# Kernel optimization log

Hardware: AMD Instinct MI355X
Metric: run time of the kernel (lower is better)

The kernel has to match this reference:

```python
import jax, jax.numpy as jnp
import numpy as np
import math

H = 16
LN_EPS = 1e-5


def setup_inputs() -> dict:
    key = jax.random.key(0)
    ks = jax.random.split(key, 12)
    D = 1024
    F = T = 2048
    S = 512
    inp = {
        "hidden_states": jax.random.normal(ks[0], (S, D), jnp.float32),
        "fpos": jax.random.randint(ks[1], (F,), 0, 512, jnp.int64 if jax.config.jax_enable_x64 else jnp.int32).astype(jnp.int32),
        "tpos": jax.random.randint(ks[2], (T,), 0, 512, jnp.int32),
        "Wq": jax.random.normal(ks[3], (D, D), jnp.float32) * 0.02,
        "Wk": jax.random.normal(ks[4], (D, D), jnp.float32) * 0.02,
        "Wcb": jax.random.normal(ks[5], (D, H), jnp.float32) * 0.02,
        "Wv": jax.random.normal(ks[6], (D, D), jnp.float32) * 0.02,
        "bv": jnp.zeros((D,), jnp.float32),
        "mixing": jax.random.normal(ks[7], (H, D), jnp.float32) * 0.2,
        "Wd": jax.random.normal(ks[8], (D, D), jnp.float32) * 0.02,
        "bd": jnp.zeros((D,), jnp.float32),
        "ln_gamma": jnp.ones((D,), jnp.float32),
        "ln_beta": jnp.zeros((D,), jnp.float32),
    }
    return inp


def reference(hidden_states, fpos, tpos, Wq, Wk, Wcb, Wv, bv, mixing, Wd, bd, ln_gamma, ln_beta):
    D = hidden_states.shape[-1]
    Dh = D // H
    scale = 1.0 / math.sqrt(D / H)  # attention_head_size = dim_key_query_all / num_heads

    fidx = fpos % 512
    tidx = tpos % 512
    from_seq = hidden_states[fidx]            # [F, D]
    to_seq = hidden_states[tidx]              # [T, D]

    q = from_seq @ Wq                          # [F, D]
    k = to_seq @ Wk                            # [T, D]

    # per-head query mixing: mixed_query[h, f, d] = q[f, d] * mixing[h, d]
    mixed_q = q[None, :, :] * mixing[:, None, :]          # [H, F, D]
    scores = jnp.einsum('hfd,td->hft', mixed_q, k)        # [H, F, T]

    # content bias: [T, H] -> broadcast over queries as [H, 1, T]
    cb = (to_seq @ Wcb).T                                 # [H, T]
    scores = (scores + cb[:, None, :]) * scale

    probs = jax.nn.softmax(scores, axis=-1)               # [H, F, T]

    v = (to_seq @ Wv + bv).reshape(-1, H, Dh).transpose(1, 0, 2)  # [H, T, Dh]
    ctx = jnp.matmul(probs, v)                             # [H, F, Dh]
    ctx = ctx.transpose(1, 0, 2).reshape(-1, D)            # [F, D]

    out = ctx @ Wd + bd                                    # [F, D]
    res = from_seq + out

    mu = jnp.mean(res, axis=-1, keepdims=True)
    var = jnp.var(res, axis=-1, keepdims=True)
    normed = (res - mu) / jnp.sqrt(var + LN_EPS)
    return normed * ln_gamma + ln_beta
```

## Files before the change

### kernel.cpp

```cpp
#include <hip/hip_runtime.h>
#include <stdint.h>
#include <math.h>

typedef float    f32x4 __attribute__((ext_vector_type(4)));
typedef float    f32x2 __attribute__((ext_vector_type(2)));
typedef short    s16x8 __attribute__((ext_vector_type(8)));
typedef short    s16x4 __attribute__((ext_vector_type(4)));
typedef unsigned u32x4 __attribute__((ext_vector_type(4)));

#define SCALE_LOG2E 0.1803368751839806f

__device__ __forceinline__ float bf2f(short s) {
  unsigned u = ((unsigned)(unsigned short)s) << 16;
  return __builtin_bit_cast(float, u);
}
__device__ __forceinline__ short f2bf(float f) {
  unsigned u = __builtin_bit_cast(unsigned, f);
  u = u + 0x7fffu + ((u >> 16) & 1u);
  return (short)(u >> 16);
}
__device__ __forceinline__ unsigned cvtpk(float lo, float hi) {
  unsigned r;
  asm("v_cvt_pk_bf16_f32 %0, %1, %2" : "=v"(r) : "v"(lo), "v"(hi));
  return r;
}
__device__ __forceinline__ void g2l16(const void* g, void* l) {
  __builtin_amdgcn_global_load_lds((const __attribute__((address_space(1))) void*)g,
                                   (__attribute__((address_space(3))) void*)l,
                                   16, 0, 0);
}
#define BARRIER() do { __builtin_amdgcn_s_barrier(); __builtin_amdgcn_sched_barrier(0); } while (0)
#define VMCNT(N)  asm volatile("s_waitcnt vmcnt(" #N ")" ::: "memory")
#define MFMA(a, b, c) __builtin_amdgcn_mfma_f32_16x16x32_bf16(a, b, c, 0, 0, 0)

__global__ void wtrans_kernel(const float* __restrict__ Wq, const float* __restrict__ Wk,
                              const float* __restrict__ Wv, const float* __restrict__ Wd,
                              short* __restrict__ WqT, short* __restrict__ WkT,
                              short* __restrict__ WvT, short* __restrict__ WdT) {
  __shared__ float tile[64][65];
  const float* src; short* dst;
  switch (blockIdx.z) {
    case 0: src = Wq; dst = WqT; break;
    case 1: src = Wk; dst = WkT; break;
    case 2: src = Wv; dst = WvT; break;
    default: src = Wd; dst = WdT; break;
  }
  int k0 = blockIdx.y * 64;
  int n0 = blockIdx.x * 64;
  int tid = threadIdx.x;
#pragma unroll
  for (int p = 0; p < 4; ++p) {
    int idx = p * 1024 + tid * 4;
    int r = idx >> 6, c = idx & 63;
    f32x4 v = *(const f32x4*)(src + (size_t)(k0 + r) * 1024 + n0 + c);
    tile[r][c + 0] = v[0]; tile[r][c + 1] = v[1];
    tile[r][c + 2] = v[2]; tile[r][c + 3] = v[3];
  }
  __syncthreads();
#pragma unroll
  for (int p = 0; p < 2; ++p) {
    int idx = p * 2048 + tid * 8;
    int r = idx >> 6, c = idx & 63;
    s16x8 o;
#pragma unroll
    for (int i = 0; i < 8; ++i) o[i] = f2bf(tile[c + i][r]);
    *(s16x8*)(dst + (size_t)(n0 + r) * 1024 + k0 + c) = o;
  }
}

__global__ void smallconv_kernel(const float* __restrict__ Wcb, const float* __restrict__ mixing,
                                 short* __restrict__ WcbT, short* __restrict__ mixbf) {
  int idx = blockIdx.x * 256 + threadIdx.x;
  if (idx < 16384) {
    int h = idx >> 10, d = idx & 1023;
    WcbT[idx] = f2bf(Wcb[d * 16 + h]);
  } else {
    int j = idx - 16384;
    mixbf[j] = f2bf(mixing[j] * SCALE_LOG2E);
  }
}

__global__ void gather_kernel(const float* __restrict__ hidden, const int* __restrict__ fpos,
                              const int* __restrict__ tpos, float* __restrict__ from_f,
                              short* __restrict__ from_bf, short* __restrict__ to_bf) {
  int row = blockIdx.x;
  int c = threadIdx.x * 4;
  if (blockIdx.y == 0) {
    int src = fpos[row] & 511;
    f32x4 v = *(const f32x4*)(hidden + (size_t)src * 1024 + c);
    *(f32x4*)(from_f + (size_t)row * 1024 + c) = v;
    s16x4 o;
#pragma unroll
    for (int i = 0; i < 4; ++i) o[i] = f2bf(v[i]);
    *(s16x4*)(from_bf + (size_t)row * 1024 + c) = o;
  } else {
    int src = tpos[row] & 511;
    f32x4 v = *(const f32x4*)(hidden + (size_t)src * 1024 + c);
    s16x4 o;
#pragma unroll
    for (int i = 0; i < 4; ++i) o[i] = f2bf(v[i]);
    *(s16x4*)(to_bf + (size_t)row * 1024 + c) = o;
  }
}

__global__ __launch_bounds__(256, 2)
void qkv_gemm(const short* __restrict__ from_bf, const short* __restrict__ to_bf,
              const short* __restrict__ WqT, const short* __restrict__ WkT,
              const short* __restrict__ WvT, const float* __restrict__ bv,
              short* __restrict__ q_swz, short* __restrict__ k_swz, short* __restrict__ vTs) {
  __shared__ __align__(16) short As[128][64];
  __shared__ __align__(16) short Bs[128][64];
  int mode = blockIdx.z;
  const short* A = (mode == 0) ? from_bf : to_bf;
  const short* B = (mode == 0) ? WqT : (mode == 1) ? WkT : WvT;
  int m0 = blockIdx.x * 128, n0 = blockIdx.y * 128;
  int tid = threadIdx.x;
  int w = tid >> 6, l = tid & 63;
  int wr = w >> 1, wc = w & 1;
  f32x4 acc[4][4] = {};
  for (int k0 = 0; k0 < 1024; k0 += 64) {
    __syncthreads();
#pragma unroll
    for (int i = 0; i < 4; ++i) {
      int off = i * 4096 + tid * 16;
      int r = off >> 7, cb_ = off & 127;
      g2l16(A + ((size_t)(m0 + r) << 10) + k0 + (cb_ >> 1), (short*)As + (off >> 1));
      g2l16(B + ((size_t)(n0 + r) << 10) + k0 + (cb_ >> 1), (short*)Bs + (off >> 1));
    }
    __syncthreads();
#pragma unroll
    for (int ks = 0; ks < 2; ++ks) {
      s16x8 af[4], bfr[4];
#pragma unroll
      for (int m = 0; m < 4; ++m)
        af[m] = *(const s16x8*)&As[wr * 64 + m * 16 + (l & 15)][ks * 32 + (l >> 4) * 8];
#pragma unroll
      for (int n = 0; n < 4; ++n)
        bfr[n] = *(const s16x8*)&Bs[wc * 64 + n * 16 + (l & 15)][ks * 32 + (l >> 4) * 8];
#pragma unroll
      for (int m = 0; m < 4; ++m)
#pragma unroll
        for (int n = 0; n < 4; ++n)
          acc[m][n] = MFMA(af[m], bfr[n], acc[m][n]);
    }
  }
  int lr = (l >> 4) * 4, lc = l & 15;
#pragma unroll
  for (int m = 0; m < 4; ++m)
#pragma unroll
    for (int n = 0; n < 4; ++n) {
      int row = m0 + wr * 64 + m * 16 + lr;
      int col = n0 + wc * 64 + n * 16 + lc;
      if (mode == 0) {
#pragma unroll
        for (int r = 0; r < 4; ++r) {
          int rr = row + r;
          q_swz[(size_t)rr * 1024 + (col ^ ((rr & 7) << 3))] = f2bf(acc[m][n][r]);
        }
      } else if (mode == 1) {
#pragma unroll
        for (int r = 0; r < 4; ++r) {
          int rr = row + r;
          k_swz[(size_t)rr * 1024 + (col ^ ((rr & 7) << 3))] = f2bf(acc[m][n][r]);
        }
      } else {
        float b = bv[col];
#pragma unroll
        for (int r = 0; r < 4; ++r) {
          int rr = row + r;
          int tsw = rr ^ ((col & 7) << 3);
          vTs[(size_t)col * 2048 + tsw] = f2bf(acc[m][n][r] + b);
        }
      }
    }
}

__global__ __launch_bounds__(256, 2)
void gemm_out(const short* __restrict__ A, const short* __restrict__ B,
              const float* __restrict__ bias, const float* __restrict__ resid,
              float* __restrict__ Cout) {
  __shared__ __align__(16) short As[128][64];
  __shared__ __align__(16) short Bs[128][64];
  int m0 = blockIdx.x * 128, n0 = blockIdx.y * 128;
  int tid = threadIdx.x;
  int w = tid >> 6, l = tid & 63;
  int wr = w >> 1, wc = w & 1;
  f32x4 acc[4][4] = {};
  for (int k0 = 0; k0 < 1024; k0 += 64) {
    __syncthreads();
#pragma unroll
    for (int i = 0; i < 4; ++i) {
      int off = i * 4096 + tid * 16;
      int r = off >> 7, cb_ = off & 127;
      g2l16(A + ((size_t)(m0 + r) << 10) + k0 + (cb_ >> 1), (short*)As + (off >> 1));
      g2l16(B + ((size_t)(n0 + r) << 10) + k0 + (cb_ >> 1), (short*)Bs + (off >> 1));
    }
    __syncthreads();
#pragma unroll
    for (int ks = 0; ks < 2; ++ks) {
      s16x8 af[4], bfr[4];
#pragma unroll
      for (int m = 0; m < 4; ++m)
        af[m] = *(const s16x8*)&As[wr * 64 + m * 16 + (l & 15)][ks * 32 + (l >> 4) * 8];
#pragma unroll
      for (int n = 0; n < 4; ++n)
        bfr[n] = *(const s16x8*)&Bs[wc * 64 + n * 16 + (l & 15)][ks * 32 + (l >> 4) * 8];
#pragma unroll
      for (int m = 0; m < 4; ++m)
#pragma unroll
        for (int n = 0; n < 4; ++n)
          acc[m][n] = MFMA(af[m], bfr[n], acc[m][n]);
    }
  }
  int lr = (l >> 4) * 4, lc = l & 15;
#pragma unroll
  for (int m = 0; m < 4; ++m)
#pragma unroll
    for (int n = 0; n < 4; ++n) {
      int row = m0 + wr * 64 + m * 16 + lr;
      int col = n0 + wc * 64 + n * 16 + lc;
      float b = bias[col];
#pragma unroll
      for (int r = 0; r < 4; ++r)
        Cout[(size_t)(row + r) * 1024 + col] = acc[m][n][r] + b + resid[(size_t)(row + r) * 1024 + col];
    }
}

__global__ void cb_kernel(const short* __restrict__ to_bf, const short* __restrict__ WcbT,
                          float* __restrict__ cbv) {
  __shared__ short Wl[16 * 1024];
  int tid = threadIdx.x;
  for (int i = tid; i < 2048; i += 256)
    ((s16x8*)Wl)[i] = ((const s16x8*)WcbT)[i];
  __syncthreads();
  int w = tid >> 6, l = tid & 63;
  int t = blockIdx.x * 4 + w;
  const s16x8* xr = (const s16x8*)(to_bf + ((size_t)t << 10) + l * 16);
  s16x8 x0 = xr[0], x1 = xr[1];
  float xf[16];
#pragma unroll
  for (int i = 0; i < 8; ++i) { xf[i] = bf2f(x0[i]); xf[8 + i] = bf2f(x1[i]); }
#pragma unroll
  for (int h = 0; h < 16; ++h) {
    const s16x8* wr_ = (const s16x8*)(Wl + h * 1024 + l * 16);
    s16x8 w0 = wr_[0], w1 = wr_[1];
    float acc = 0.f;
#pragma unroll
    for (int i = 0; i < 8; ++i) { acc += xf[i] * bf2f(w0[i]); acc += xf[8 + i] * bf2f(w1[i]); }
#pragma unroll
    for (int s = 32; s; s >>= 1) acc += __shfl_xor(acc, s);
    if (l == 0) cbv[(size_t)h * 2048 + t] = acc * SCALE_LOG2E;
  }
}

__global__ void qmix_kernel(const short* __restrict__ q_swz, const short* __restrict__ mixbf,
                            short* __restrict__ qmix) {
  int f = blockIdx.x, h = blockIdx.y;
  int c = threadIdx.x * 8;
  int fs = (f & 7) << 3;
  s16x8 qv = *(const s16x8*)(q_swz + ((size_t)f << 10) + c);
  s16x8 mv = *(const s16x8*)(mixbf + ((size_t)h << 10) + (c ^ fs));
  u32x4 o;
#pragma unroll
  for (int e2 = 0; e2 < 4; ++e2)
    o[e2] = cvtpk(bf2f(qv[2 * e2]) * bf2f(mv[2 * e2]),
                  bf2f(qv[2 * e2 + 1]) * bf2f(mv[2 * e2 + 1]));
  *(s16x8*)(qmix + (((size_t)h * 2048 + f) << 10) + c) = __builtin_bit_cast(s16x8, o);
}

template <bool QMIX>
__global__ __launch_bounds__(512, 2)
void attn_kernel(const short* __restrict__ qsrc, const short* __restrict__ k_swz,
                 const short* __restrict__ vTs, const short* __restrict__ mixbf,
                 const float* __restrict__ cbg, float* __restrict__ ctxp,
                 f32x2* __restrict__ mlb) {
  __shared__ __align__(16) char smem[120832];
  char* qmA = smem;          char* qmB = smem + 32768;
  char* ktA = smem + 65536;  char* ktB = smem + 81920;
  char* vt  = smem + 98304;
  float* cbl  = (float*)(smem + 114688);
  short* mixl = (short*)(smem + 118784);
  const int f0 = blockIdx.x * 256, h = blockIdx.y, ts = blockIdx.z;
  const int tb = ts << 10;
  const int tid = threadIdx.x, w = tid >> 6, l = tid & 63;
  const int lr = l >> 4, lc = l & 15;
  const int swz = (lc & 7) << 4;

  for (int i = tid; i < 1024; i += 512) cbl[i] = cbg[h * 2048 + tb + i];
  if (!QMIX)
    for (int i = tid; i < 128; i += 512)
      ((s16x8*)mixl)[i] = ((const s16x8*)(mixbf + ((size_t)h << 10)))[i];
  __syncthreads();

  const short* qrow = QMIX ? qsrc + (((size_t)h * 2048 + f0) << 10)
                           : qsrc + ((size_t)f0 << 10);

#define ISSUE_QK(qmb, ktb, k0e, trow0)                                                     \
  do {                                                                                     \
    _Pragma("unroll") for (int i_ = 0; i_ < 4; ++i_) {                                     \
      int off_ = i_ * 8192 + tid * 16;                                                     \
      g2l16(qrow + ((size_t)(off_ >> 7) << 10) + (k0e) + ((off_ & 127) >> 1),              \
            (qmb) + off_);                                                                 \
    }                                                                                      \
    _Pragma("unroll") for (int i_ = 0; i_ < 2; ++i_) {                                     \
      int off_ = i_ * 8192 + tid * 16;                                                     \
      g2l16(k_swz + ((size_t)((trow0) + (off_ >> 7)) << 10) + (k0e) + ((off_ & 127) >> 1), \
            (ktb) + off_);                                                                 \
    }                                                                                      \
  } while (0)

  ISSUE_QK(qmA, ktA, 0, tb);

  float m_run[8], l_run[8];
#pragma unroll
  for (int s2 = 0; s2 < 8; ++s2) { m_run[s2] = -1e30f; l_run[s2] = 0.f; }
  f32x4 ctx[2][4] = {};

  for (int t0 = 0; t0 < 1024; t0 += 128) {
#pragma unroll
    for (int i = 0; i < 2; ++i) {
      int off = i * 8192 + tid * 16;
      g2l16(vTs + ((size_t)(h * 64 + (off >> 8)) << 11) + tb + t0 + ((off & 255) >> 1), vt + off);
    }
    f32x4 sacc[2][8] = {};
    for (int c = 0; c < 16; ++c) {
      char* qmb = (c & 1) ? qmB : qmA;
      char* ktb = (c & 1) ? ktB : ktA;
      if (c < 15) {
        ISSUE_QK((c & 1) ? qmA : qmB, (c & 1) ? ktA : ktB, (c + 1) * 64, tb + t0);
      } else if (t0 < 896) {
        ISSUE_QK(qmA, ktA, 0, tb + t0 + 128);
      }
      if (c == 0) { VMCNT(8); }
      else if (c == 15 && t0 == 896) { VMCNT(0); }
      else { VMCNT(6); }
      BARRIER();
      const int k0b = c << 7;
#pragma unroll
      for (int ks = 0; ks < 2; ++ks) {
        int xr = ks * 64 + lr * 16;
        s16x8 af0, af1;
        if (QMIX) {
          af0 = *(const s16x8*)(qmb + ((w * 32 + lc) << 7) + (xr ^ swz));
          af1 = *(const s16x8*)(qmb + ((w * 32 + 16 + lc) << 7) + (xr ^ swz));
        } else {
          s16x8 mx = *(const s16x8*)((char*)mixl + k0b + xr);
          s16x8 qv = *(const s16x8*)(qmb + ((w * 32 + lc) << 7) + (xr ^ swz));
          s16x8 qw = *(const s16x8*)(qmb + ((w * 32 + 16 + lc) << 7) + (xr ^ swz));
          u32x4 a0u, a1u;
#pragma unroll
          for (int e2 = 0; e2 < 4; ++e2) {
            float m0 = bf2f(mx[2 * e2]), m1 = bf2f(mx[2 * e2 + 1]);
            a0u[e2] = cvtpk(bf2f(qv[2 * e2]) * m0, bf2f(qv[2 * e2 + 1]) * m1);
            a1u[e2] = cvtpk(bf2f(qw[2 * e2]) * m0, bf2f(qw[2 * e2 + 1]) * m1);
          }
          af0 = __builtin_bit_cast(s16x8, a0u);
          af1 = __builtin_bit_cast(s16x8, a1u);
        }
        __builtin_amdgcn_s_setprio(1);
#pragma unroll
        for (int n = 0; n < 8; ++n) {
          s16x8 bfr = *(const s16x8*)(ktb + ((n * 16 + lc) << 7) + (xr ^ swz));
          sacc[0][n] = MFMA(af0, bfr, sacc[0][n]);
          sacc[1][n] = MFMA(af1, bfr, sacc[1][n]);
        }
        __builtin_amdgcn_s_setprio(0);
      }
      BARRIER();
    }
    float pm[8];
#pragma unroll
    for (int s2 = 0; s2 < 8; ++s2) pm[s2] = -1e30f;
#pragma unroll
    for (int m = 0; m < 2; ++m)
#pragma unroll
      for (int n = 0; n < 8; ++n) {
        float cbv = cbl[t0 + n * 16 + lc];
#pragma unroll
        for (int r = 0; r < 4; ++r) {
          float s = sacc[m][n][r] + cbv;
          sacc[m][n][r] = s;
          pm[m * 4 + r] = fmaxf(pm[m * 4 + r], s);
        }
      }
#pragma unroll
    for (int s_ = 1; s_ < 16; s_ <<= 1)
#pragma unroll
      for (int s2 = 0; s2 < 8; ++s2) pm[s2] = fmaxf(pm[s2], __shfl_xor(pm[s2], s_));
    float tsum[8];
#pragma unroll
    for (int s2 = 0; s2 < 8; ++s2) {
      float mnew = fmaxf(m_run[s2], pm[s2]);
      float corr = exp2f(m_run[s2] - mnew);
      m_run[s2] = mnew; l_run[s2] *= corr; tsum[s2] = 0.f;
      int m = s2 >> 2, r = s2 & 3;
#pragma unroll
      for (int n2 = 0; n2 < 4; ++n2) ctx[m][n2][r] *= corr;
    }
#pragma unroll
    for (int m = 0; m < 2; ++m)
#pragma unroll
      for (int n = 0; n < 8; ++n)
#pragma unroll
        for (int r = 0; r < 4; ++r) {
          float e = exp2f(sacc[m][n][r] - m_run[m * 4 + r]);
          sacc[m][n][r] = e;
          tsum[m * 4 + r] += e;
        }
#pragma unroll
    for (int s_ = 1; s_ < 16; s_ <<= 1)
#pragma unroll
      for (int s2 = 0; s2 < 8; ++s2) tsum[s2] += __shfl_xor(tsum[s2], s_);
#pragma unroll
    for (int s2 = 0; s2 < 8; ++s2) l_run[s2] += tsum[s2];
    char* ptw = qmB + w * 4096;
#pragma unroll
    for (int hh = 0; hh < 2; ++hh) {
#pragma unroll
      for (int m = 0; m < 2; ++m)
#pragma unroll
        for (int nn = 0; nn < 4; ++nn)
#pragma unroll
          for (int r = 0; r < 4; ++r) {
            int row = m * 16 + lr * 4 + r;
            *(short*)(ptw + (row << 7) + ((((nn * 16 + lc) << 1)) ^ ((row & 7) << 4))) =
                f2bf(sacc[m][hh * 4 + nn][r]);
          }
#pragma unroll
      for (int ks = 0; ks < 2; ++ks) {
        s16x8 paf0 = *(const s16x8*)(ptw + (lc << 7) + ((ks * 64 + lr * 16) ^ swz));
        s16x8 paf1 = *(const s16x8*)(ptw + ((16 + lc) << 7) + ((ks * 64 + lr * 16) ^ swz));
#pragma unroll
        for (int n2 = 0; n2 < 4; ++n2) {
          s16x8 vb = *(const s16x8*)(vt + ((n2 * 16 + lc) << 8) +
                                     ((hh * 128 + ks * 64 + lr * 16) ^ swz));
          ctx[0][n2] = MFMA(paf0, vb, ctx[0][n2]);
          ctx[1][n2] = MFMA(paf1, vb, ctx[1][n2]);
        }
      }
    }
    BARRIER();
  }
  const int pb = (h * 2 + ts) * 2048;
#pragma unroll
  for (int m = 0; m < 2; ++m)
#pragma unroll
    for (int n2 = 0; n2 < 4; ++n2)
#pragma unroll
      for (int r = 0; r < 4; ++r) {
        int f = f0 + w * 32 + m * 16 + lr * 4 + r;
        ctxp[((size_t)(pb + f) << 6) + n2 * 16 + lc] = ctx[m][n2][r];
      }
  if (lc == 0) {
#pragma unroll
    for (int s2 = 0; s2 < 8; ++s2) {
      int f = f0 + w * 32 + (s2 >> 2) * 16 + lr * 4 + (s2 & 3);
      f32x2 v; v[0] = m_run[s2]; v[1] = l_run[s2];
      mlb[pb + f] = v;
    }
  }
#undef ISSUE_QK
}

__global__ void combine_kernel(const float* __restrict__ ctxp, const f32x2* __restrict__ mlb,
                               short* __restrict__ ctx_bf) {
  int f = blockIdx.x, tid = threadIdx.x;
  int h = tid >> 4, d4 = (tid & 15) * 4;
  f32x2 a = mlb[(h * 2 + 0) * 2048 + f];
  f32x2 b = mlb[(h * 2 + 1) * 2048 + f];
  float m = fmaxf(a[0], b[0]);
  float e0 = exp2f(a[0] - m), e1 = exp2f(b[0] - m);
  float inv = 1.f / (a[1] * e0 + b[1] * e1);
  f32x4 c0 = *(const f32x4*)(ctxp + (((size_t)(h * 2 + 0) * 2048 + f) << 6) + d4);
  f32x4 c1 = *(const f32x4*)(ctxp + (((size_t)(h * 2 + 1) * 2048 + f) << 6) + d4);
  s16x4 o;
#pragma unroll
  for (int i = 0; i < 4; ++i) o[i] = f2bf((c0[i] * e0 + c1[i] * e1) * inv);
  *(s16x4*)(ctx_bf + ((size_t)f << 10) + h * 64 + d4) = o;
}

__global__ void ln_kernel(const float* __restrict__ res, const float* __restrict__ gamma,
                          const float* __restrict__ beta, float* __restrict__ out) {
  int row = blockIdx.x, tid = threadIdx.x;
  f32x4 x = *(const f32x4*)(res + ((size_t)row << 10) + tid * 4);
  float s = x[0] + x[1] + x[2] + x[3];
  float s2 = x[0] * x[0] + x[1] * x[1] + x[2] * x[2] + x[3] * x[3];
#pragma unroll
  for (int m = 1; m < 64; m <<= 1) { s += __shfl_xor(s, m); s2 += __shfl_xor(s2, m); }
  __shared__ float red[8];
  int w = tid >> 6, l = tid & 63;
  if (l == 0) { red[w] = s; red[4 + w] = s2; }
  __syncthreads();
  s = red[0] + red[1] + red[2] + red[3];
  s2 = red[4] + red[5] + red[6] + red[7];
  float mu = s * (1.f / 1024.f);
  float var = s2 * (1.f / 1024.f) - mu * mu;
  float rstd = rsqrtf(var + 1e-5f);
  f32x4 o;
#pragma unroll
  for (int i = 0; i < 4; ++i)
    o[i] = (x[i] - mu) * rstd * gamma[tid * 4 + i] + beta[tid * 4 + i];
  *(f32x4*)(out + ((size_t)row << 10) + tid * 4) = o;
}

extern "C" void kernel_launch(void* const* d_in, const int* in_sizes, int n_in,
                              void* d_out, int out_size, void* d_ws, size_t ws_size,
                              hipStream_t stream) {
  const float* hidden = (const float*)d_in[0];
  const int*   fpos   = (const int*)d_in[1];
  const int*   tpos   = (const int*)d_in[2];
  const float* Wq     = (const float*)d_in[3];
  const float* Wk     = (const float*)d_in[4];
  const float* Wcb    = (const float*)d_in[5];
  const float* Wv     = (const float*)d_in[6];
  const float* bv     = (const float*)d_in[7];
  const float* mixing = (const float*)d_in[8];
  const float* Wd     = (const float*)d_in[9];
  const float* bd     = (const float*)d_in[10];
  const float* gamma  = (const float*)d_in[11];
  const float* beta   = (const float*)d_in[12];

  char* p = (char*)d_ws;
  auto alloc = [&](size_t bytes) { char* r = p; p += (bytes + 255) & ~(size_t)255; return r; };
  float* from_f  = (float*)alloc((size_t)2048 * 1024 * 4);
  short* from_bf = (short*)alloc((size_t)2048 * 1024 * 2);
  short* to_bf   = (short*)alloc((size_t)2048 * 1024 * 2);
  short* WqT     = (short*)alloc((size_t)1024 * 1024 * 2);
  short* WkT     = (short*)alloc((size_t)1024 * 1024 * 2);
  short* WvT     = (short*)alloc((size_t)1024 * 1024 * 2);
  short* WdT     = (short*)alloc((size_t)1024 * 1024 * 2);
  short* WcbT    = (short*)alloc((size_t)16 * 1024 * 2);
  short* mixbf   = (short*)alloc((size_t)16 * 1024 * 2);
  short* q_swz   = (short*)alloc((size_t)2048 * 1024 * 2);
  short* k_swz   = (short*)alloc((size_t)2048 * 1024 * 2);
  short* vTs     = (short*)alloc((size_t)1024 * 2048 * 2);
  float* cbb     = (float*)alloc((size_t)16 * 2048 * 4);
  short* ctx_bf  = (short*)alloc((size_t)2048 * 1024 * 2);
  float* ctxp    = (float*)alloc((size_t)32 * 2048 * 64 * 4);
  f32x2* mlb     = (f32x2*)alloc((size_t)32 * 2048 * 8);
  size_t used = (size_t)(p - (char*)d_ws);
  short* qmixb = (short*)p;
  bool use_qmix = ws_size >= used + (size_t)16 * 2048 * 1024 * 2;

  wtrans_kernel<<<dim3(16, 16, 4), 256, 0, stream>>>(Wq, Wk, Wv, Wd, WqT, WkT, WvT, WdT);
  smallconv_kernel<<<128, 256, 0, stream>>>(Wcb, mixing, WcbT, mixbf);
  gather_kernel<<<dim3(2048, 2), 256, 0, stream>>>(hidden, fpos, tpos, from_f, from_bf, to_bf);
  qkv_gemm<<<dim3(16, 8, 3), 256, 0, stream>>>(from_bf, to_bf, WqT, WkT, WvT, bv,
                                               q_swz, k_swz, vTs);
  cb_kernel<<<512, 256, 0, stream>>>(to_bf, WcbT, cbb);
  if (use_qmix) {
    qmix_kernel<<<dim3(2048, 16), 128, 0, stream>>>(q_swz, mixbf, qmixb);
    attn_kernel<true><<<dim3(8, 16, 2), 512, 0, stream>>>(qmixb, k_swz, vTs, mixbf, cbb, ctxp, mlb);
  } else {
    attn_kernel<false><<<dim3(8, 16, 2), 512, 0, stream>>>(q_swz, k_swz, vTs, mixbf, cbb, ctxp, mlb);
  }
  combine_kernel<<<2048, 256, 0, stream>>>(ctxp, mlb, ctx_bf);
  gemm_out<<<dim3(16, 8), 256, 0, stream>>>(ctx_bf, WdT, bd, from_f, (float*)d_out);
  ln_kernel<<<2048, 256, 0, stream>>>((float*)d_out, gamma, beta, (float*)d_out);
}
```

Measured before the change: 350.7 us.

## Use FP8 MFMA for attention QK scores and split keys four ways

Attention scores are now computed with FP8 MFMA. Mixed queries and keys are pre-quantized to FP8 with power-of-two scales (64 and 4), which are undone by multiplying by 1/256. The key dimension is split into four partitions instead of two to give 256 blocks, with smaller shared memory allowing four blocks per CU, and combine merges four partials. The V layout is permuted so the P·V stage packs probabilities with cvt_pk in 32-column chunks. This halves the Q/K bytes moved and doubles MFMA rate, at the cost of FP8 precision in scores and an extra key-conversion kernel.

```diff
diff --git a/kernel.cpp b/kernel.cpp
--- a/kernel.cpp
+++ b/kernel.cpp
@@ -6,7 +6,7 @@
 typedef float    f32x2 __attribute__((ext_vector_type(2)));
 typedef short    s16x8 __attribute__((ext_vector_type(8)));
 typedef short    s16x4 __attribute__((ext_vector_type(4)));
-typedef unsigned u32x4 __attribute__((ext_vector_type(4)));
+typedef unsigned u32x2 __attribute__((ext_vector_type(2)));
 
 #define SCALE_LOG2E 0.1803368751839806f
 
@@ -31,7 +31,13 @@
 }
 #define BARRIER() do { __builtin_amdgcn_s_barrier(); __builtin_amdgcn_sched_barrier(0); } while (0)
 #define VMCNT(N)  asm volatile("s_waitcnt vmcnt(" #N ")" ::: "memory")
-#define MFMA(a, b, c) __builtin_amdgcn_mfma_f32_16x16x32_bf16(a, b, c, 0, 0, 0)
+#define LGKM0()   do { asm volatile("s_waitcnt lgkmcnt(0)" ::: "memory"); __builtin_amdgcn_sched_barrier(0); } while (0)
+#define MFMA(a, b, c)  __builtin_amdgcn_mfma_f32_16x16x32_bf16(a, b, c, 0, 0, 0)
+#define MFMA8(a, b, c) __builtin_amdgcn_mfma_f32_16x16x32_fp8_fp8(a, b, c, 0, 0, 0)
+
+__device__ __forceinline__ int pi32(int t) {
+  return (t & ~31) | ((t & 15) << 1) | ((t >> 4) & 1);
+}
 
 __global__ void wtrans_kernel(const float* __restrict__ Wq, const float* __restrict__ Wk,
                               const float* __restrict__ Wv, const float* __restrict__ Wd,
@@ -76,7 +82,7 @@
     WcbT[idx] = f2bf(Wcb[d * 16 + h]);
   } else {
     int j = idx - 16384;
-    mixbf[j] = f2bf(mixing[j] * SCALE_LOG2E);
+    mixbf[j] = f2bf(mixing[j] * (SCALE_LOG2E * 64.0f));
   }
 }
 
@@ -168,11 +174,262 @@
 #pragma unroll
         for (int r = 0; r < 4; ++r) {
           int rr = row + r;
-          int tsw = rr ^ ((col & 7) << 3);
+          int tsw = pi32(rr) ^ ((col & 7) << 3);
           vTs[(size_t)col * 2048 + tsw] = f2bf(acc[m][n][r] + b);
         }
       }
     }
+}
+
+__global__ void k8_kernel(const short* __restrict__ k_swz, unsigned char* __restrict__ k8) {
+  int gid = blockIdx.x * 256 + threadIdx.x;
+  int row = gid >> 7, c = (gid & 127) * 8;
+  s16x8 v = *(const s16x8*)(k_swz + ((size_t)row << 10) + c);
+  unsigned lo = 0, hi = 0;
+  lo = __builtin_amdgcn_cvt_pk_fp8_f32(bf2f(v[0]) * 4.f, bf2f(v[1]) * 4.f, lo, false);
+  lo = __builtin_amdgcn_cvt_pk_fp8_f32(bf2f(v[2]) * 4.f, bf2f(v[3]) * 4.f, lo, true);
+  hi = __builtin_amdgcn_cvt_pk_fp8_f32(bf2f(v[4]) * 4.f, bf2f(v[5]) * 4.f, hi, false);
+  hi = __builtin_amdgcn_cvt_pk_fp8_f32(bf2f(v[6]) * 4.f, bf2f(v[7]) * 4.f, hi, true);
+  u32x2 o; o[0] = lo; o[1] = hi;
+  *(u32x2*)(k8 + ((size_t)row << 10) + c) = o;
+}
+
+__global__ void qmix8_kernel(const short* __restrict__ q_swz, const short* __restrict__ mixbf,
+                             unsigned char* __restrict__ qm8) {
+  int f = blockIdx.x, h = blockIdx.y;
+  int c = threadIdx.x * 8;
+  int fs = (f & 7) << 3;
+  s16x8 qv = *(const s16x8*)(q_swz + ((size_t)f << 10) + c);
+  s16x8 mv = *(const s16x8*)(mixbf + ((size_t)h << 10) + (c ^ fs));
+  float p[8];
+#pragma unroll
+  for (int i = 0; i < 8; ++i) p[i] = bf2f(qv[i]) * bf2f(mv[i]);
+  unsigned lo = 0, hi = 0;
+  lo = __builtin_amdgcn_cvt_pk_fp8_f32(p[0], p[1], lo, false);
+  lo = __builtin_amdgcn_cvt_pk_fp8_f32(p[2], p[3], lo, true);
+  hi = __builtin_amdgcn_cvt_pk_fp8_f32(p[4], p[5], hi, false);
+  hi = __builtin_amdgcn_cvt_pk_fp8_f32(p[6], p[7], hi, true);
+  u32x2 o; o[0] = lo; o[1] = hi;
+  *(u32x2*)(qm8 + (((size_t)h * 2048 + f) << 10) + c) = o;
+}
+
+__global__ void cb_kernel(const short* __restrict__ to_bf, const short* __restrict__ WcbT,
+                          float* __restrict__ cbv) {
+  __shared__ short Wl[16 * 1024];
+  int tid = threadIdx.x;
+  for (int i = tid; i < 2048; i += 256)
+    ((s16x8*)Wl)[i] = ((const s16x8*)WcbT)[i];
+  __syncthreads();
+  int w = tid >> 6, l = tid & 63;
+  int t = blockIdx.x * 4 + w;
+  const s16x8* xr = (const s16x8*)(to_bf + ((size_t)t << 10) + l * 16);
+  s16x8 x0 = xr[0], x1 = xr[1];
+  float xf[16];
+#pragma unroll
+  for (int i = 0; i < 8; ++i) { xf[i] = bf2f(x0[i]); xf[8 + i] = bf2f(x1[i]); }
+#pragma unroll
+  for (int h = 0; h < 16; ++h) {
+    const s16x8* wr_ = (const s16x8*)(Wl + h * 1024 + l * 16);
+    s16x8 w0 = wr_[0], w1 = wr_[1];
+    float acc = 0.f;
+#pragma unroll
+    for (int i = 0; i < 8; ++i) { acc += xf[i] * bf2f(w0[i]); acc += xf[8 + i] * bf2f(w1[i]); }
+#pragma unroll
+    for (int s = 32; s; s >>= 1) acc += __shfl_xor(acc, s);
+    if (l == 0) cbv[(size_t)h * 2048 + t] = acc * SCALE_LOG2E;
+  }
+}
+
+__global__ __launch_bounds__(512, 4)
+void attn_kernel(const unsigned char* __restrict__ qm8, const unsigned char* __restrict__ k8,
+                 const short* __restrict__ vTs, const float* __restrict__ cbg,
+                 float* __restrict__ ctxp, f32x2* __restrict__ mlb) {
+  __shared__ __align__(16) char smem[67584];
+  char* qmA = smem;          char* qmB = smem + 16384;
+  char* ktA = smem + 32768;  char* ktB = smem + 40960;
+  char* vt  = smem + 49152;
+  float* cbl = (float*)(smem + 65536);
+  const int f0 = blockIdx.x * 256, h = blockIdx.y, ts = blockIdx.z;
+  const int tb = ts << 9;
+  const int tid = threadIdx.x, w = tid >> 6, l = tid & 63;
+  const int lr = l >> 4, lc = l & 15;
+  const int swz8 = (lc & 7) << 3;
+  cbl[tid & 511] = cbg[h * 2048 + tb + (tid & 511)];
+  const unsigned char* qbase = qm8 + (((size_t)h * 2048 + f0) << 10);
+
+#define ISSUE_QK(qmb, ktb, k0e, trow0)                                                      \
+  do {                                                                                      \
+    _Pragma("unroll") for (int i_ = 0; i_ < 2; ++i_) {                                      \
+      int off_ = i_ * 8192 + tid * 16;                                                      \
+      g2l16(qbase + ((size_t)(off_ >> 6) << 10) + (k0e) + (off_ & 63), (qmb) + off_);       \
+    }                                                                                       \
+    {                                                                                       \
+      int off_ = tid * 16;                                                                  \
+      g2l16(k8 + ((size_t)((trow0) + (off_ >> 6)) << 10) + (k0e) + (off_ & 63),             \
+            (ktb) + off_);                                                                  \
+    }                                                                                       \
+  } while (0)
+
+  ISSUE_QK(qmA, ktA, 0, tb);
+
+  float m_run[8], l_run[8];
+#pragma unroll
+  for (int s2 = 0; s2 < 8; ++s2) { m_run[s2] = -1e30f; l_run[s2] = 0.f; }
+  f32x4 ctx[2][4] = {};
+
+  for (int t0 = 0; t0 < 512; t0 += 128) {
+#pragma unroll
+    for (int i = 0; i < 2; ++i) {
+      int off = i * 8192 + tid * 16;
+      g2l16(vTs + (((size_t)(h * 64 + (off >> 8))) << 11) + tb + t0 + ((off & 255) >> 1),
+            vt + off);
+    }
+    f32x4 sacc[2][8] = {};
+    for (int c = 0; c < 16; ++c) {
+      char* qmb = (c & 1) ? qmB : qmA;
+      char* ktb = (c & 1) ? ktB : ktA;
+      if (c < 15) {
+        ISSUE_QK((c & 1) ? qmA : qmB, (c & 1) ? ktA : ktB, (c + 1) * 64, tb + t0);
+      } else if (t0 < 384) {
+        ISSUE_QK(qmA, ktA, 0, tb + t0 + 128);
+      }
+      if (c == 0) { VMCNT(5); }
+      else if (c == 15 && t0 == 384) { VMCNT(0); }
+      else { VMCNT(3); }
+      BARRIER();
+#pragma unroll
+      for (int ks = 0; ks < 2; ++ks) {
+        int xr = (ks * 32 + lr * 8) ^ swz8;
+        long af0 = *(const long*)(qmb + ((w * 32 + lc) << 6) + xr);
+        long af1 = *(const long*)(qmb + ((w * 32 + 16 + lc) << 6) + xr);
+        __builtin_amdgcn_s_setprio(1);
+#pragma unroll
+        for (int n = 0; n < 8; ++n) {
+          long bfr = *(const long*)(ktb + ((n * 16 + lc) << 6) + xr);
+          sacc[0][n] = MFMA8(af0, bfr, sacc[0][n]);
+          sacc[1][n] = MFMA8(af1, bfr, sacc[1][n]);
+        }
+        __builtin_amdgcn_s_setprio(0);
+      }
+      BARRIER();
+    }
+    float pm[8];
+#pragma unroll
+    for (int s2 = 0; s2 < 8; ++s2) pm[s2] = -1e30f;
+#pragma unroll
+    for (int m = 0; m < 2; ++m)
+#pragma unroll
+      for (int n = 0; n < 8; ++n) {
+        float cbv = cbl[t0 + n * 16 + lc];
+#pragma unroll
+        for (int r = 0; r < 4; ++r) {
+          float s = fmaf(sacc[m][n][r], 0.00390625f, cbv);
+          sacc[m][n][r] = s;
+          pm[m * 4 + r] = fmaxf(pm[m * 4 + r], s);
+        }
+      }
+#pragma unroll
+    for (int s_ = 1; s_ < 16; s_ <<= 1)
+#pragma unroll
+      for (int s2 = 0; s2 < 8; ++s2) pm[s2] = fmaxf(pm[s2], __shfl_xor(pm[s2], s_));
+    float tsum[8];
+#pragma unroll
+    for (int s2 = 0; s2 < 8; ++s2) {
+      float mnew = fmaxf(m_run[s2], pm[s2]);
+      float corr = exp2f(m_run[s2] - mnew);
+      m_run[s2] = mnew; l_run[s2] *= corr; tsum[s2] = 0.f;
+      int m = s2 >> 2, r = s2 & 3;
+#pragma unroll
+      for (int n2 = 0; n2 < 4; ++n2) ctx[m][n2][r] *= corr;
+    }
+#pragma unroll
+    for (int m = 0; m < 2; ++m)
+#pragma unroll
+      for (int n = 0; n < 8; ++n)
+#pragma unroll
+        for (int r = 0; r < 4; ++r) {
+          float e = exp2f(sacc[m][n][r] - m_run[m * 4 + r]);
+          sacc[m][n][r] = e;
+          tsum[m * 4 + r] += e;
+        }
+#pragma unroll
+    for (int s_ = 1; s_ < 16; s_ <<= 1)
+#pragma unroll
+      for (int s2 = 0; s2 < 8; ++s2) tsum[s2] += __shfl_xor(tsum[s2], s_);
+#pragma unroll
+    for (int s2 = 0; s2 < 8; ++s2) l_run[s2] += tsum[s2];
+    char* ptw = qmB + (w << 11);
+#pragma unroll
+    for (int qq = 0; qq < 4; ++qq) {
+      if (qq) { LGKM0(); }
+#pragma unroll
+      for (int m = 0; m < 2; ++m)
+#pragma unroll
+        for (int r = 0; r < 4; ++r) {
+          int row = m * 16 + lr * 4 + r;
+          unsigned pk = cvtpk(sacc[m][2 * qq][r], sacc[m][2 * qq + 1][r]);
+          *(unsigned*)(ptw + (row << 6) + ((lc << 2) ^ ((row & 3) << 4))) = pk;
+        }
+      LGKM0();
+      s16x8 paf0 = *(const s16x8*)(ptw + (lc << 6) + ((lr * 16) ^ ((lc & 3) << 4)));
+      s16x8 paf1 = *(const s16x8*)(ptw + ((16 + lc) << 6) + ((lr * 16) ^ ((lc & 3) << 4)));
+#pragma unroll
+      for (int n2 = 0; n2 < 4; ++n2) {
+        s16x8 vb = *(const s16x8*)(vt + ((n2 * 16 + lc) << 8) +
+                                   ((qq * 64 + lr * 16) ^ ((lc & 7) << 4)));
+        ctx[0][n2] = MFMA(paf0, vb, ctx[0][n2]);
+        ctx[1][n2] = MFMA(paf1, vb, ctx[1][n2]);
+      }
+    }
+    BARRIER();
+  }
+  const int pb = (h * 4 + ts) * 2048;
+#pragma unroll
+  for (int m = 0; m < 2; ++m)
+#pragma unroll
+    for (int n2 = 0; n2 < 4; ++n2)
+#pragma unroll
+      for (int r = 0; r < 4; ++r) {
+        int f = f0 + w * 32 + m * 16 + lr * 4 + r;
+        ctxp[((size_t)(pb + f) << 6) + n2 * 16 + lc] = ctx[m][n2][r];
+      }
+  if (lc == 0) {
+#pragma unroll
+    for (int s2 = 0; s2 < 8; ++s2) {
+      int f = f0 + w * 32 + (s2 >> 2) * 16 + lr * 4 + (s2 & 3);
+      f32x2 v; v[0] = m_run[s2]; v[1] = l_run[s2];
+      mlb[pb + f] = v;
+    }
+  }
+#undef ISSUE_QK
+}
+
+__global__ void combine_kernel(const float* __restrict__ ctxp, const f32x2* __restrict__ mlb,
+                               short* __restrict__ ctx_bf) {
+  int f = blockIdx.x, tid = threadIdx.x;
+  int h = tid >> 4, d4 = (tid & 15) * 4;
+  f32x2 ml[4];
+  float mx = -1e30f;
+#pragma unroll
+  for (int p = 0; p < 4; ++p) {
+    ml[p] = mlb[(h * 4 + p) * 2048 + f];
+    mx = fmaxf(mx, ml[p][0]);
+  }
+  float e[4], L = 0.f;
+#pragma unroll
+  for (int p = 0; p < 4; ++p) { e[p] = exp2f(ml[p][0] - mx); L += ml[p][1] * e[p]; }
+  float inv = 1.f / L;
+  f32x4 s = {};
+#pragma unroll
+  for (int p = 0; p < 4; ++p) {
+    f32x4 cp = *(const f32x4*)(ctxp + (((size_t)(h * 4 + p) * 2048 + f) << 6) + d4);
+#pragma unroll
+    for (int i = 0; i < 4; ++i) s[i] += cp[i] * e[p];
+  }
+  s16x4 o;
+#pragma unroll
+  for (int i = 0; i < 4; ++i) o[i] = f2bf(s[i] * inv);
+  *(s16x4*)(ctx_bf + ((size_t)f << 10) + h * 64 + d4) = o;
 }
 
 __global__ __launch_bounds__(256, 2)
@@ -224,259 +481,6 @@
       for (int r = 0; r < 4; ++r)
         Cout[(size_t)(row + r) * 1024 + col] = acc[m][n][r] + b + resid[(size_t)(row + r) * 1024 + col];
     }
-}
-
-__global__ void cb_kernel(const short* __restrict__ to_bf, const short* __restrict__ WcbT,
-                          float* __restrict__ cbv) {
-  __shared__ short Wl[16 * 1024];
-  int tid = threadIdx.x;
-  for (int i = tid; i < 2048; i += 256)
-    ((s16x8*)Wl)[i] = ((const s16x8*)WcbT)[i];
-  __syncthreads();
-  int w = tid >> 6, l = tid & 63;
-  int t = blockIdx.x * 4 + w;
-  const s16x8* xr = (const s16x8*)(to_bf + ((size_t)t << 10) + l * 16);
-  s16x8 x0 = xr[0], x1 = xr[1];
-  float xf[16];
-#pragma unroll
-  for (int i = 0; i < 8; ++i) { xf[i] = bf2f(x0[i]); xf[8 + i] = bf2f(x1[i]); }
-#pragma unroll
-  for (int h = 0; h < 16; ++h) {
-    const s16x8* wr_ = (const s16x8*)(Wl + h * 1024 + l * 16);
-    s16x8 w0 = wr_[0], w1 = wr_[1];
-    float acc = 0.f;
-#pragma unroll
-    for (int i = 0; i < 8; ++i) { acc += xf[i] * bf2f(w0[i]); acc += xf[8 + i] * bf2f(w1[i]); }
-#pragma unroll
-    for (int s = 32; s; s >>= 1) acc += __shfl_xor(acc, s);
-    if (l == 0) cbv[(size_t)h * 2048 + t] = acc * SCALE_LOG2E;
-  }
-}
-
-__global__ void qmix_kernel(const short* __restrict__ q_swz, const short* __restrict__ mixbf,
-                            short* __restrict__ qmix) {
-  int f = blockIdx.x, h = blockIdx.y;
-  int c = threadIdx.x * 8;
-  int fs = (f & 7) << 3;
-  s16x8 qv = *(const s16x8*)(q_swz + ((size_t)f << 10) + c);
-  s16x8 mv = *(const s16x8*)(mixbf + ((size_t)h << 10) + (c ^ fs));
-  u32x4 o;
-#pragma unroll
-  for (int e2 = 0; e2 < 4; ++e2)
-    o[e2] = cvtpk(bf2f(qv[2 * e2]) * bf2f(mv[2 * e2]),
-                  bf2f(qv[2 * e2 + 1]) * bf2f(mv[2 * e2 + 1]));
-  *(s16x8*)(qmix + (((size_t)h * 2048 + f) << 10) + c) = __builtin_bit_cast(s16x8, o);
-}
-
-template <bool QMIX>
-__global__ __launch_bounds__(512, 2)
-void attn_kernel(const short* __restrict__ qsrc, const short* __restrict__ k_swz,
-                 const short* __restrict__ vTs, const short* __restrict__ mixbf,
-                 const float* __restrict__ cbg, float* __restrict__ ctxp,
-                 f32x2* __restrict__ mlb) {
-  __shared__ __align__(16) char smem[120832];
-  char* qmA = smem;          char* qmB = smem + 32768;
-  char* ktA = smem + 65536;  char* ktB = smem + 81920;
-  char* vt  = smem + 98304;
-  float* cbl  = (float*)(smem + 114688);
-  short* mixl = (short*)(smem + 118784);
-  const int f0 = blockIdx.x * 256, h = blockIdx.y, ts = blockIdx.z;
-  const int tb = ts << 10;
-  const int tid = threadIdx.x, w = tid >> 6, l = tid & 63;
-  const int lr = l >> 4, lc = l & 15;
-  const int swz = (lc & 7) << 4;
-
-  for (int i = tid; i < 1024; i += 512) cbl[i] = cbg[h * 2048 + tb + i];
-  if (!QMIX)
-    for (int i = tid; i < 128; i += 512)
-      ((s16x8*)mixl)[i] = ((const s16x8*)(mixbf + ((size_t)h << 10)))[i];
-  __syncthreads();
-
-  const short* qrow = QMIX ? qsrc + (((size_t)h * 2048 + f0) << 10)
-                           : qsrc + ((size_t)f0 << 10);
-
-#define ISSUE_QK(qmb, ktb, k0e, trow0)                                                     \
-  do {                                                                                     \
-    _Pragma("unroll") for (int i_ = 0; i_ < 4; ++i_) {                                     \
-      int off_ = i_ * 8192 + tid * 16;                                                     \
-      g2l16(qrow + ((size_t)(off_ >> 7) << 10) + (k0e) + ((off_ & 127) >> 1),              \
-            (qmb) + off_);                                                                 \
-    }                                                                                      \
-    _Pragma("unroll") for (int i_ = 0; i_ < 2; ++i_) {                                     \
-      int off_ = i_ * 8192 + tid * 16;                                                     \
-      g2l16(k_swz + ((size_t)((trow0) + (off_ >> 7)) << 10) + (k0e) + ((off_ & 127) >> 1), \
-            (ktb) + off_);                                                                 \
-    }                                                                                      \
-  } while (0)
-
-  ISSUE_QK(qmA, ktA, 0, tb);
-
-  float m_run[8], l_run[8];
-#pragma unroll
-  for (int s2 = 0; s2 < 8; ++s2) { m_run[s2] = -1e30f; l_run[s2] = 0.f; }
-  f32x4 ctx[2][4] = {};
-
-  for (int t0 = 0; t0 < 1024; t0 += 128) {
-#pragma unroll
-    for (int i = 0; i < 2; ++i) {
-      int off = i * 8192 + tid * 16;
-      g2l16(vTs + ((size_t)(h * 64 + (off >> 8)) << 11) + tb + t0 + ((off & 255) >> 1), vt + off);
-    }
-    f32x4 sacc[2][8] = {};
-    for (int c = 0; c < 16; ++c) {
-      char* qmb = (c & 1) ? qmB : qmA;
-      char* ktb = (c & 1) ? ktB : ktA;
-      if (c < 15) {
-        ISSUE_QK((c & 1) ? qmA : qmB, (c & 1) ? ktA : ktB, (c + 1) * 64, tb + t0);
-      } else if (t0 < 896) {
-        ISSUE_QK(qmA, ktA, 0, tb + t0 + 128);
-      }
-      if (c == 0) { VMCNT(8); }
-      else if (c == 15 && t0 == 896) { VMCNT(0); }
-      else { VMCNT(6); }
-      BARRIER();
-      const int k0b = c << 7;
-#pragma unroll
-      for (int ks = 0; ks < 2; ++ks) {
-        int xr = ks * 64 + lr * 16;
-        s16x8 af0, af1;
-        if (QMIX) {
-          af0 = *(const s16x8*)(qmb + ((w * 32 + lc) << 7) + (xr ^ swz));
-          af1 = *(const s16x8*)(qmb + ((w * 32 + 16 + lc) << 7) + (xr ^ swz));
-        } else {
-          s16x8 mx = *(const s16x8*)((char*)mixl + k0b + xr);
-          s16x8 qv = *(const s16x8*)(qmb + ((w * 32 + lc) << 7) + (xr ^ swz));
-          s16x8 qw = *(const s16x8*)(qmb + ((w * 32 + 16 + lc) << 7) + (xr ^ swz));
-          u32x4 a0u, a1u;
-#pragma unroll
-          for (int e2 = 0; e2 < 4; ++e2) {
-            float m0 = bf2f(mx[2 * e2]), m1 = bf2f(mx[2 * e2 + 1]);
-            a0u[e2] = cvtpk(bf2f(qv[2 * e2]) * m0, bf2f(qv[2 * e2 + 1]) * m1);
-            a1u[e2] = cvtpk(bf2f(qw[2 * e2]) * m0, bf2f(qw[2 * e2 + 1]) * m1);
-          }
-          af0 = __builtin_bit_cast(s16x8, a0u);
-          af1 = __builtin_bit_cast(s16x8, a1u);
-        }
-        __builtin_amdgcn_s_setprio(1);
-#pragma unroll
-        for (int n = 0; n < 8; ++n) {
-          s16x8 bfr = *(const s16x8*)(ktb + ((n * 16 + lc) << 7) + (xr ^ swz));
-          sacc[0][n] = MFMA(af0, bfr, sacc[0][n]);
-          sacc[1][n] = MFMA(af1, bfr, sacc[1][n]);
-        }
-        __builtin_amdgcn_s_setprio(0);
-      }
-      BARRIER();
-    }
-    float pm[8];
-#pragma unroll
-    for (int s2 = 0; s2 < 8; ++s2) pm[s2] = -1e30f;
-#pragma unroll
-    for (int m = 0; m < 2; ++m)
-#pragma unroll
-      for (int n = 0; n < 8; ++n) {
-        float cbv = cbl[t0 + n * 16 + lc];
-#pragma unroll
-        for (int r = 0; r < 4; ++r) {
-          float s = sacc[m][n][r] + cbv;
-          sacc[m][n][r] = s;
-          pm[m * 4 + r] = fmaxf(pm[m * 4 + r], s);
-        }
-      }
-#pragma unroll
-    for (int s_ = 1; s_ < 16; s_ <<= 1)
-#pragma unroll
-      for (int s2 = 0; s2 < 8; ++s2) pm[s2] = fmaxf(pm[s2], __shfl_xor(pm[s2], s_));
-    float tsum[8];
-#pragma unroll
-    for (int s2 = 0; s2 < 8; ++s2) {
-      float mnew = fmaxf(m_run[s2], pm[s2]);
-      float corr = exp2f(m_run[s2] - mnew);
-      m_run[s2] = mnew; l_run[s2] *= corr; tsum[s2] = 0.f;
-      int m = s2 >> 2, r = s2 & 3;
-#pragma unroll
-      for (int n2 = 0; n2 < 4; ++n2) ctx[m][n2][r] *= corr;
-    }
-#pragma unroll
-    for (int m = 0; m < 2; ++m)
-#pragma unroll
-      for (int n = 0; n < 8; ++n)
-#pragma unroll
-        for (int r = 0; r < 4; ++r) {
-          float e = exp2f(sacc[m][n][r] - m_run[m * 4 + r]);
-          sacc[m][n][r] = e;
-          tsum[m * 4 + r] += e;
-        }
-#pragma unroll
-    for (int s_ = 1; s_ < 16; s_ <<= 1)
-#pragma unroll
-      for (int s2 = 0; s2 < 8; ++s2) tsum[s2] += __shfl_xor(tsum[s2], s_);
-#pragma unroll
-    for (int s2 = 0; s2 < 8; ++s2) l_run[s2] += tsum[s2];
-    char* ptw = qmB + w * 4096;
-#pragma unroll
-    for (int hh = 0; hh < 2; ++hh) {
-#pragma unroll
-      for (int m = 0; m < 2; ++m)
-#pragma unroll
-        for (int nn = 0; nn < 4; ++nn)
-#pragma unroll
-          for (int r = 0; r < 4; ++r) {
-            int row = m * 16 + lr * 4 + r;
-            *(short*)(ptw + (row << 7) + ((((nn * 16 + lc) << 1)) ^ ((row & 7) << 4))) =
-                f2bf(sacc[m][hh * 4 + nn][r]);
-          }
-#pragma unroll
-      for (int ks = 0; ks < 2; ++ks) {
-        s16x8 paf0 = *(const s16x8*)(ptw + (lc << 7) + ((ks * 64 + lr * 16) ^ swz));
-        s16x8 paf1 = *(const s16x8*)(ptw + ((16 + lc) << 7) + ((ks * 64 + lr * 16) ^ swz));
-#pragma unroll
-        for (int n2 = 0; n2 < 4; ++n2) {
-          s16x8 vb = *(const s16x8*)(vt + ((n2 * 16 + lc) << 8) +
-                                     ((hh * 128 + ks * 64 + lr * 16) ^ swz));
-          ctx[0][n2] = MFMA(paf0, vb, ctx[0][n2]);
-          ctx[1][n2] = MFMA(paf1, vb, ctx[1][n2]);
-        }
-      }
-    }
-    BARRIER();
-  }
-  const int pb = (h * 2 + ts) * 2048;
-#pragma unroll
-  for (int m = 0; m < 2; ++m)
-#pragma unroll
-    for (int n2 = 0; n2 < 4; ++n2)
-#pragma unroll
-      for (int r = 0; r < 4; ++r) {
-        int f = f0 + w * 32 + m * 16 + lr * 4 + r;
-        ctxp[((size_t)(pb + f) << 6) + n2 * 16 + lc] = ctx[m][n2][r];
-      }
-  if (lc == 0) {
-#pragma unroll
-    for (int s2 = 0; s2 < 8; ++s2) {
-      int f = f0 + w * 32 + (s2 >> 2) * 16 + lr * 4 + (s2 & 3);
-      f32x2 v; v[0] = m_run[s2]; v[1] = l_run[s2];
-      mlb[pb + f] = v;
-    }
-  }
-#undef ISSUE_QK
-}
-
-__global__ void combine_kernel(const float* __restrict__ ctxp, const f32x2* __restrict__ mlb,
-                               short* __restrict__ ctx_bf) {
-  int f = blockIdx.x, tid = threadIdx.x;
-  int h = tid >> 4, d4 = (tid & 15) * 4;
-  f32x2 a = mlb[(h * 2 + 0) * 2048 + f];
-  f32x2 b = mlb[(h * 2 + 1) * 2048 + f];
-  float m = fmaxf(a[0], b[0]);
-  float e0 = exp2f(a[0] - m), e1 = exp2f(b[0] - m);
-  float inv = 1.f / (a[1] * e0 + b[1] * e1);
-  f32x4 c0 = *(const f32x4*)(ctxp + (((size_t)(h * 2 + 0) * 2048 + f) << 6) + d4);
-  f32x4 c1 = *(const f32x4*)(ctxp + (((size_t)(h * 2 + 1) * 2048 + f) << 6) + d4);
-  s16x4 o;
-#pragma unroll
-  for (int i = 0; i < 4; ++i) o[i] = f2bf((c0[i] * e0 + c1[i] * e1) * inv);
-  *(s16x4*)(ctx_bf + ((size_t)f << 10) + h * 64 + d4) = o;
 }
 
 __global__ void ln_kernel(const float* __restrict__ res, const float* __restrict__ gamma,
@@ -534,26 +538,22 @@
   short* q_swz   = (short*)alloc((size_t)2048 * 1024 * 2);
   short* k_swz   = (short*)alloc((size_t)2048 * 1024 * 2);
   short* vTs     = (short*)alloc((size_t)1024 * 2048 * 2);
+  unsigned char* k8  = (unsigned char*)alloc((size_t)2048 * 1024);
+  unsigned char* qm8 = (unsigned char*)alloc((size_t)16 * 2048 * 1024);
   float* cbb     = (float*)alloc((size_t)16 * 2048 * 4);
   short* ctx_bf  = (short*)alloc((size_t)2048 * 1024 * 2);
-  float* ctxp    = (float*)alloc((size_t)32 * 2048 * 64 * 4);
-  f32x2* mlb     = (f32x2*)alloc((size_t)32 * 2048 * 8);
-  size_t used = (size_t)(p - (char*)d_ws);
-  short* qmixb = (short*)p;
-  bool use_qmix = ws_size >= used + (size_t)16 * 2048 * 1024 * 2;
+  float* ctxp    = (float*)alloc((size_t)64 * 2048 * 64 * 4);
+  f32x2* mlb     = (f32x2*)alloc((size_t)64 * 2048 * 8);
 
   wtrans_kernel<<<dim3(16, 16, 4), 256, 0, stream>>>(Wq, Wk, Wv, Wd, WqT, WkT, WvT, WdT);
   smallconv_kernel<<<128, 256, 0, stream>>>(Wcb, mixing, WcbT, mixbf);
   gather_kernel<<<dim3(2048, 2), 256, 0, stream>>>(hidden, fpos, tpos, from_f, from_bf, to_bf);
   qkv_gemm<<<dim3(16, 8, 3), 256, 0, stream>>>(from_bf, to_bf, WqT, WkT, WvT, bv,
                                                q_swz, k_swz, vTs);
+  k8_kernel<<<1024, 256, 0, stream>>>(k_swz, k8);
   cb_kernel<<<512, 256, 0, stream>>>(to_bf, WcbT, cbb);
-  if (use_qmix) {
-    qmix_kernel<<<dim3(2048, 16), 128, 0, stream>>>(q_swz, mixbf, qmixb);
-    attn_kernel<true><<<dim3(8, 16, 2), 512, 0, stream>>>(qmixb, k_swz, vTs, mixbf, cbb, ctxp, mlb);
-  } else {
-    attn_kernel<false><<<dim3(8, 16, 2), 512, 0, stream>>>(q_swz, k_swz, vTs, mixbf, cbb, ctxp, mlb);
-  }
+  qmix8_kernel<<<dim3(2048, 16), 128, 0, stream>>>(q_swz, mixbf, qm8);
+  attn_kernel<<<dim3(8, 16, 4), 512, 0, stream>>>(qm8, k8, vTs, cbb, ctxp, mlb);
   combine_kernel<<<2048, 256, 0, stream>>>(ctxp, mlb, ctx_bf);
   gemm_out<<<dim3(16, 8), 256, 0, stream>>>(ctx_bf, WdT, bd, from_f, (float*)d_out);
   ln_kernel<<<2048, 256, 0, stream>>>((float*)d_out, gamma, beta, (float*)d_out);
```

After: 393.8 us. 1.12x slower.
